# Kernel optimization log

Hardware: AMD Instinct MI355X
Metric: run time of the kernel (lower is better)

The kernel has to match this reference:

```python
import jax, jax.numpy as jnp
import numpy as np

N_NODES = 100000
N_EDGES = 1600000
N_GRAPHS = 1000
X_S = 128
HID = 64


def setup_inputs() -> dict:
    key = jax.random.key(0)
    ks = jax.random.split(key, 12)
    x = jax.random.normal(ks[0], (N_NODES, X_S), dtype=jnp.float32)
    edge_index = jax.random.randint(ks[1], (2, N_EDGES), 0, N_NODES, dtype=jnp.int64)
    batch = jnp.sort(jax.random.randint(ks[2], (N_NODES,), 0, N_GRAPHS, dtype=jnp.int64))
    def lin(k, fin, fout):
        s = 1.0 / np.sqrt(fin)
        kw, kb = jax.random.split(k)
        W = jax.random.uniform(kw, (fin, fout), minval=-s, maxval=s, dtype=jnp.float32)
        b = jax.random.uniform(kb, (fout,), minval=-s, maxval=s, dtype=jnp.float32)
        return W, b
    W1, b1 = lin(ks[3], X_S, HID)
    W2, b2 = lin(ks[4], HID, HID)
    W3, b3 = lin(ks[5], HID, HID)
    Wf, bf = lin(ks[6], HID, 10)
    Wl, bl = lin(ks[7], 10, 1)
    eps1 = jnp.float32(0.37)
    eps2 = jnp.float32(0.72)
    eps3 = jnp.float32(0.11)
    return {"x": x, "edge_index": edge_index, "batch": batch,
            "W1": W1, "b1": b1, "W2": W2, "b2": b2, "W3": W3, "b3": b3,
            "Wf": Wf, "bf": bf, "Wl": Wl, "bl": bl,
            "eps1": eps1, "eps2": eps2, "eps3": eps3}


def _gin_conv(h, src, dst, eps, W, b):
    # GIN: nn((1+eps)*x_i + sum_{j in N(i)} x_j); messages flow src -> dst
    agg = jax.ops.segment_sum(h[src], dst, num_segments=N_NODES)  # [N, d]
    return ((1.0 + eps) * h + agg) @ W + b


def reference(x, edge_index, batch, W1, b1, W2, b2, W3, b3, Wf, bf, Wl, bl,
              eps1, eps2, eps3):
    src, dst = edge_index[0], edge_index[1]
    h = jax.nn.relu(_gin_conv(x, src, dst, eps1, W1, b1))
    h = jax.nn.relu(_gin_conv(h, src, dst, eps2, W2, b2))
    h = jax.nn.relu(_gin_conv(h, src, dst, eps3, W3, b3))
    # global_mean_pool over graph ids
    sums = jax.ops.segment_sum(h, batch, num_segments=N_GRAPHS)        # [G, 64]
    cnts = jax.ops.segment_sum(jnp.ones((N_NODES,), h.dtype), batch,
                               num_segments=N_GRAPHS)                   # [G]
    pooled = sums / jnp.maximum(cnts, 1.0)[:, None]
    out = jax.nn.relu(pooled @ Wf + bf) @ Wl + bl                       # [G, 1]
    return out
```

## Files before the change

### kernel.cpp

```cpp
#include <hip/hip_runtime.h>

#define N_NODES 100000
#define N_EDGES 1600000
#define N_GRAPHS 1000

#define NB_C 391
#define B1   1024
#define CHUNK_E ((N_EDGES + B1 - 1) / B1)
#define MTOT (NB_C * B1)
#define STG_MAX 4736

typedef unsigned int uint32;
typedef unsigned short ushort16;
typedef __attribute__((ext_vector_type(8))) short short8;
typedef __attribute__((ext_vector_type(4))) float f32x4;

static __device__ __forceinline__ ushort16 f2bf(float f) {
    uint32 u = __float_as_uint(f);
    u += 0x7fffu + ((u >> 16) & 1u);
    return (ushort16)(u >> 16);
}
static __device__ __forceinline__ uint32 pk2(float a, float b) {
    return (uint32)f2bf(a) | ((uint32)f2bf(b) << 16);
}
static __device__ __forceinline__ void bf2x(uint32 v, float& lo, float& hi) {
    lo = __uint_as_float(v << 16);
    hi = __uint_as_float(v & 0xffff0000u);
}
static __device__ __forceinline__ void acc8(float* a, uint4 v) {
    float lo, hi;
    bf2x(v.x, lo, hi); a[0] += lo; a[1] += hi;
    bf2x(v.y, lo, hi); a[2] += lo; a[3] += hi;
    bf2x(v.z, lo, hi); a[4] += lo; a[5] += hi;
    bf2x(v.w, lo, hi); a[6] += lo; a[7] += hi;
}

union CV8 { uint4 u; short8 s; };

__global__ __launch_bounds__(256) void convw_kernel(
    const float* __restrict__ W1, const float* __restrict__ W2,
    const float* __restrict__ W3,
    ushort16* __restrict__ W1t, ushort16* __restrict__ W2t,
    ushort16* __restrict__ W3t)
{
    int t = threadIdx.x;
    if (blockIdx.x == 0) {
        for (int i = t; i < 64 * 128; i += 256) {
            int j = i >> 7, k = i & 127;
            W1t[i] = f2bf(W1[k * 64 + j]);
        }
    } else if (blockIdx.x == 1) {
        for (int i = t; i < 64 * 64; i += 256) {
            int j = i >> 6, k = i & 63;
            W2t[i] = f2bf(W2[k * 64 + j]);
        }
    } else {
        for (int i = t; i < 64 * 64; i += 256) {
            int j = i >> 6, k = i & 63;
            W3t[i] = f2bf(W3[k * 64 + j]);
        }
    }
}


__global__ __launch_bounds__(256) void count_kernel(
    const int* __restrict__ dst, int* __restrict__ M)
{
    __shared__ int cnt[NB_C];
    int b = blockIdx.x, t = threadIdx.x;
    for (int q = t; q < NB_C; q += 256) cnt[q] = 0;
    __syncthreads();
    int e0 = b * CHUNK_E;
    int e1 = e0 + CHUNK_E; if (e1 > N_EDGES) e1 = N_EDGES;
    for (int e = e0 + t; e < e1; e += 256)
        atomicAdd(&cnt[dst[e] >> 8], 1);
    __syncthreads();
    for (int q = t; q < NB_C; q += 256) M[q * B1 + b] = cnt[q];
}

#define SCAN_B 1024
#define SCAN_NBLK (MTOT / SCAN_B)

__global__ __launch_bounds__(256) void scanA_kernel(
    const int* __restrict__ in, int* __restrict__ excl, int* __restrict__ bsum)
{
    __shared__ int s[256];
    int b = blockIdx.x, t = threadIdx.x;
    int base = b * SCAN_B + t * 4;
    int v[4];
#pragma unroll
    for (int i = 0; i < 4; ++i) v[i] = (base + i < MTOT) ? in[base + i] : 0;
    int tsum = v[0] + v[1] + v[2] + v[3];
    s[t] = tsum;
    __syncthreads();
    for (int off = 1; off < 256; off <<= 1) {
        int x = (t >= off) ? s[t - off] : 0;
        __syncthreads();
        s[t] += x;
        __syncthreads();
    }
    int run = s[t] - tsum;
#pragma unroll
    for (int i = 0; i < 4; ++i) {
        if (base + i < MTOT) excl[base + i] = run;
        run += v[i];
    }
    if (t == 255) bsum[b] = s[255];
}

__global__ __launch_bounds__(512) void scanB_kernel(int* __restrict__ bsum)
{
    __shared__ int s[512];
    int t = threadIdx.x;
    int v = (t < SCAN_NBLK) ? bsum[t] : 0;
    s[t] = v;
    __syncthreads();
    for (int off = 1; off < 512; off <<= 1) {
        int x = (t >= off) ? s[t - off] : 0;
        __syncthreads();
        s[t] += x;
        __syncthreads();
    }
    if (t < SCAN_NBLK) bsum[t] = s[t] - v;
}

__global__ __launch_bounds__(256) void scanC_kernel(
    const int* __restrict__ excl, const int* __restrict__ bsum,
    int* __restrict__ out)
{
    int b = blockIdx.x, t = threadIdx.x;
    int add = bsum[b];
    int base = b * SCAN_B + t * 4;
#pragma unroll
    for (int i = 0; i < 4; ++i)
        if (base + i < MTOT) out[base + i] = excl[base + i] + add;
}

__global__ __launch_bounds__(256) void scatter_kernel(
    const int* __restrict__ src, const int* __restrict__ dst,
    const int* __restrict__ Ms, uint32* __restrict__ tmp)
{
    __shared__ int cnt[NB_C];
    __shared__ int loc[NB_C];
    __shared__ int cur[NB_C];
    __shared__ int msb[NB_C];
    __shared__ int ssum[256];
    __shared__ uint32 staged[CHUNK_E];
    __shared__ unsigned short bkt[CHUNK_E];
    int b = blockIdx.x, t = threadIdx.x;
    int e0 = b * CHUNK_E;
    int e1 = e0 + CHUNK_E; if (e1 > N_EDGES) e1 = N_EDGES;
    int n = e1 - e0;

    for (int q = t; q < NB_C; q += 256) {
        cnt[q] = 0;
        msb[q] = Ms[q * B1 + b];
    }
    __syncthreads();
    for (int e = e0 + t; e < e1; e += 256)
        atomicAdd(&cnt[dst[e] >> 8], 1);
    __syncthreads();
    int q0 = 2 * t, q1 = 2 * t + 1;
    int c0 = (q0 < NB_C) ? cnt[q0] : 0;
    int c1 = (q1 < NB_C) ? cnt[q1] : 0;
    int pairsum = c0 + c1;
    ssum[t] = pairsum;
    __syncthreads();
    for (int off = 1; off < 256; off <<= 1) {
        int x = (t >= off) ? ssum[t - off] : 0;
        __syncthreads();
        ssum[t] += x;
        __syncthreads();
    }
    int excl = ssum[t] - pairsum;
    if (q0 < NB_C) { loc[q0] = excl; cur[q0] = excl; }
    if (q1 < NB_C) { loc[q1] = excl + c0; cur[q1] = excl + c0; }
    __syncthreads();
    for (int e = e0 + t; e < e1; e += 256) {
        int d = dst[e];
        int q = d >> 8;
        int pos = atomicAdd(&cur[q], 1);
        staged[pos] = ((uint32)(d & 255) << 17) | (uint32)src[e];
        bkt[pos] = (unsigned short)q;
    }
    __syncthreads();
    for (int i = t; i < n; i += 256) {
        int q = bkt[i];
        tmp[msb[q] + (i - loc[q])] = staged[i];
    }
}

__global__ __launch_bounds__(256) void finalize_kernel(
    const uint32* __restrict__ tmp, const int* __restrict__ Ms,
    int* __restrict__ row_off, int* __restrict__ esrc)
{
    __shared__ int cnt[256];
    __shared__ int pref[256];
    __shared__ int cur[256];
    __shared__ uint32 stg[STG_MAX];
    int q = blockIdx.x, t = threadIdx.x;
    int start = Ms[q * B1];
    int end = (q == NB_C - 1) ? N_EDGES : Ms[(q + 1) * B1];
    int seg = end - start;

    cnt[t] = 0;
    __syncthreads();
    for (int e = start + t; e < end; e += 256)
        atomicAdd(&cnt[tmp[e] >> 17], 1);
    __syncthreads();
    pref[t] = cnt[t];
    __syncthreads();
    for (int off = 1; off < 256; off <<= 1) {
        int x = (t >= off) ? pref[t - off] : 0;
        __syncthreads();
        pref[t] += x;
        __syncthreads();
    }
    {
        int excl = pref[t] - cnt[t];
        int node = q * 256 + t;
        if (node < N_NODES) row_off[node] = start + excl;
        cur[t] = excl;
    }
    if (q == 0 && t == 0) row_off[N_NODES] = N_EDGES;
    __syncthreads();
    if (seg <= STG_MAX) {
        for (int e = start + t; e < end; e += 256) {
            uint32 u = tmp[e];
            int pos = atomicAdd(&cur[u >> 17], 1);
            stg[pos] = u & 0x1FFFFu;
        }
        __syncthreads();
        for (int i = t; i < seg; i += 256)
            esrc[start + i] = (int)stg[i];
    } else {
        for (int e = start + t; e < end; e += 256) {
            uint32 u = tmp[e];
            int pos = atomicAdd(&cur[u >> 17], 1);
            esrc[start + pos] = (int)(u & 0x1FFFFu);
        }
    }
}

__global__ __launch_bounds__(256) void gemm1_mfma_kernel(
    const float* __restrict__ x,
    const ushort16* __restrict__ Wt,
    ushort16* __restrict__ y)
{
    int lane = threadIdx.x & 63;
    int wave = threadIdx.x >> 6;
    int col = lane & 15, quad = lane >> 4;
    int node0 = blockIdx.x * 64 + wave * 16;
    int anode = node0 + col;

    short8 a[4];
    if (anode < N_NODES) {
        const float* xr = &x[(size_t)anode * 128 + quad * 8];
#pragma unroll
        for (int s = 0; s < 4; ++s) {
            float4 v0 = *(const float4*)&xr[s * 32];
            float4 v1 = *(const float4*)&xr[s * 32 + 4];
            CV8 cv;
            cv.u = make_uint4(pk2(v0.x, v0.y), pk2(v0.z, v0.w),
                              pk2(v1.x, v1.y), pk2(v1.z, v1.w));
            a[s] = cv.s;
        }
    } else {
        short8 z = {0, 0, 0, 0, 0, 0, 0, 0};
#pragma unroll
        for (int s = 0; s < 4; ++s) a[s] = z;
    }

    f32x4 acc[4];
#pragma unroll
    for (int nt = 0; nt < 4; ++nt)
#pragma unroll
        for (int r = 0; r < 4; ++r) acc[nt][r] = 0.0f;

#pragma unroll
    for (int nt = 0; nt < 4; ++nt) {
        const ushort16* wr = &Wt[(size_t)(nt * 16 + col) * 128 + quad * 8];
#pragma unroll
        for (int s = 0; s < 4; ++s) {
            short8 b = *(const short8*)&wr[s * 32];
            acc[nt] = __builtin_amdgcn_mfma_f32_16x16x32_bf16(a[s], b, acc[nt], 0, 0, 0);
        }
    }

#pragma unroll
    for (int nt = 0; nt < 4; ++nt)
#pragma unroll
        for (int r = 0; r < 4; ++r) {
            int node = node0 + quad * 4 + r;
            if (node < N_NODES)
                y[(size_t)node * 64 + nt * 16 + col] = f2bf(acc[nt][r]);
        }
}

__global__ __launch_bounds__(256) void aggregate_kernel(
    const uint4* __restrict__ y4,
    const int* __restrict__ row_off,
    const int* __restrict__ esrc,
    const float* __restrict__ b,
    const float* __restrict__ eps_p,
    uint4* __restrict__ out4)
{
    int lane = threadIdx.x & 63;
    int wave = threadIdx.x >> 6;
    int grp = lane >> 3;
    int w = lane & 7;
    int node = blockIdx.x * 32 + wave * 8 + grp;

    int s0 = row_off[node], s1 = row_off[node + 1];
    float a[8], c[8];
#pragma unroll
    for (int i = 0; i < 8; ++i) { a[i] = 0.f; c[i] = 0.f; }

    int e = s0;
    for (; e + 3 < s1; e += 4) {
        int i0 = esrc[e];
        int i1 = esrc[e + 1];
        int i2 = esrc[e + 2];
        int i3 = esrc[e + 3];
        uint4 v0 = y4[(size_t)i0 * 8 + w];
        uint4 v1 = y4[(size_t)i1 * 8 + w];
        uint4 v2 = y4[(size_t)i2 * 8 + w];
        uint4 v3 = y4[(size_t)i3 * 8 + w];
        acc8(a, v0);
        acc8(c, v1);
        acc8(a, v2);
        acc8(c, v3);
    }
    for (; e < s1; ++e) {
        uint4 v0 = y4[(size_t)esrc[e] * 8 + w];
        acc8(a, v0);
    }
#pragma unroll
    for (int i = 0; i < 8; ++i) a[i] += c[i];

    uint4 sv = y4[(size_t)node * 8 + w];
    float s[8];
    bf2x(sv.x, s[0], s[1]);
    bf2x(sv.y, s[2], s[3]);
    bf2x(sv.z, s[4], s[5]);
    bf2x(sv.w, s[6], s[7]);
    float ep1 = 1.0f + eps_p[0];
    float4 b0 = *(const float4*)&b[w * 8];
    float4 b1 = *(const float4*)&b[w * 8 + 4];
    float r0 = fmaxf(fmaf(ep1, s[0], a[0]) + b0.x, 0.0f);
    float r1 = fmaxf(fmaf(ep1, s[1], a[1]) + b0.y, 0.0f);
    float r2 = fmaxf(fmaf(ep1, s[2], a[2]) + b0.z, 0.0f);
    float r3 = fmaxf(fmaf(ep1, s[3], a[3]) + b0.w, 0.0f);
    float r4 = fmaxf(fmaf(ep1, s[4], a[4]) + b1.x, 0.0f);
    float r5 = fmaxf(fmaf(ep1, s[5], a[5]) + b1.y, 0.0f);
    float r6 = fmaxf(fmaf(ep1, s[6], a[6]) + b1.z, 0.0f);
    float r7 = fmaxf(fmaf(ep1, s[7], a[7]) + b1.w, 0.0f);
    out4[(size_t)node * 8 + w] =
        make_uint4(pk2(r0, r1), pk2(r2, r3), pk2(r4, r5), pk2(r6, r7));
}

__global__ __launch_bounds__(256) void agg_gemm_fused_kernel(
    const uint4* __restrict__ h4,
    const int* __restrict__ row_off,
    const int* __restrict__ esrc,
    const ushort16* __restrict__ Wt,
    const float* __restrict__ bias,
    const float* __restrict__ eps_p,
    ushort16* __restrict__ hout)
{
    __shared__ __align__(16) ushort16 zl[4][16][72];
    int lane = threadIdx.x & 63;
    int wave = threadIdx.x >> 6;
    int g = lane >> 2;
    int c = lane & 3;
    int node0 = blockIdx.x * 64 + wave * 16;
    if (node0 >= N_NODES) return;
    int node = node0 + g;

    int s0 = row_off[node], s1 = row_off[node + 1];
    float a[16], d[16];
#pragma unroll
    for (int i = 0; i < 16; ++i) { a[i] = 0.f; d[i] = 0.f; }

    const size_t cb = (size_t)c * 2;
    int e = s0;
    for (; e + 3 < s1; e += 4) {
        int i0 = esrc[e];
        int i1 = esrc[e + 1];
        int i2 = esrc[e + 2];
        int i3 = esrc[e + 3];
        uint4 v0a = h4[(size_t)i0 * 8 + cb], v0b = h4[(size_t)i0 * 8 + cb + 1];
        uint4 v1a = h4[(size_t)i1 * 8 + cb], v1b = h4[(size_t)i1 * 8 + cb + 1];
        uint4 v2a = h4[(size_t)i2 * 8 + cb], v2b = h4[(size_t)i2 * 8 + cb + 1];
        uint4 v3a = h4[(size_t)i3 * 8 + cb], v3b = h4[(size_t)i3 * 8 + cb + 1];
        acc8(a, v0a); acc8(a + 8, v0b);
        acc8(d, v1a); acc8(d + 8, v1b);
        acc8(a, v2a); acc8(a + 8, v2b);
        acc8(d, v3a); acc8(d + 8, v3b);
    }
    for (; e < s1; ++e) {
        int i0 = esrc[e];
        uint4 va = h4[(size_t)i0 * 8 + cb], vb = h4[(size_t)i0 * 8 + cb + 1];
        acc8(a, va); acc8(a + 8, vb);
    }
#pragma unroll
    for (int i = 0; i < 16; ++i) a[i] += d[i];

    uint4 sva = h4[(size_t)node * 8 + cb], svb = h4[(size_t)node * 8 + cb + 1];
    float s[16];
    bf2x(sva.x, s[0], s[1]);  bf2x(sva.y, s[2], s[3]);
    bf2x(sva.z, s[4], s[5]);  bf2x(sva.w, s[6], s[7]);
    bf2x(svb.x, s[8], s[9]);  bf2x(svb.y, s[10], s[11]);
    bf2x(svb.z, s[12], s[13]); bf2x(svb.w, s[14], s[15]);
    float ep1 = 1.0f + eps_p[0];
    float z[16];
#pragma unroll
    for (int i = 0; i < 16; ++i) z[i] = fmaf(ep1, s[i], a[i]);

    uint4 pA = make_uint4(pk2(z[0], z[1]), pk2(z[2], z[3]),
                          pk2(z[4], z[5]), pk2(z[6], z[7]));
    uint4 pB = make_uint4(pk2(z[8], z[9]), pk2(z[10], z[11]),
                          pk2(z[12], z[13]), pk2(z[14], z[15]));
    *(uint4*)&zl[wave][g][c * 16] = pA;
    *(uint4*)&zl[wave][g][c * 16 + 8] = pB;

    int col = lane & 15, quad = lane >> 4;
    short8 a0 = *(const short8*)&zl[wave][col][quad * 8];
    short8 a1 = *(const short8*)&zl[wave][col][32 + quad * 8];

    f32x4 acc[4];
#pragma unroll
    for (int nt = 0; nt < 4; ++nt)
#pragma unroll
        for (int r = 0; r < 4; ++r) acc[nt][r] = 0.0f;

#pragma unroll
    for (int nt = 0; nt < 4; ++nt) {
        const ushort16* wr = &Wt[(size_t)(nt * 16 + col) * 64 + quad * 8];
        short8 b0 = *(const short8*)&wr[0];
        short8 b1 = *(const short8*)&wr[32];
        acc[nt] = __builtin_amdgcn_mfma_f32_16x16x32_bf16(a0, b0, acc[nt], 0, 0, 0);
        acc[nt] = __builtin_amdgcn_mfma_f32_16x16x32_bf16(a1, b1, acc[nt], 0, 0, 0);
    }

#pragma unroll
    for (int nt = 0; nt < 4; ++nt) {
        float bl = bias[nt * 16 + col];
#pragma unroll
        for (int r = 0; r < 4; ++r) {
            int nd = node0 + quad * 4 + r;
            hout[(size_t)nd * 64 + nt * 16 + col] =
                f2bf(fmaxf(acc[nt][r] + bl, 0.0f));
        }
    }
}

__global__ __launch_bounds__(256) void pool_head_kernel(
    const uint32* __restrict__ hb,
    const int* __restrict__ batch,
    const float* __restrict__ Wf,
    const float* __restrict__ bfv,
    const float* __restrict__ Wl,
    const float* __restrict__ blv,
    float* __restrict__ out)
{
    __shared__ float red[4][64];
    __shared__ float pooled[64];
    __shared__ float hid[10];
    int g = blockIdx.x;
    int t = threadIdx.x;
    int lo = 0, hi = N_NODES;
    while (lo < hi) { int mid = (lo + hi) >> 1; if (batch[mid] < g) lo = mid + 1; else hi = mid; }
    int start = lo;
    hi = N_NODES;
    while (lo < hi) { int mid = (lo + hi) >> 1; if (batch[mid] < g + 1) lo = mid + 1; else hi = mid; }
    int end = lo;

    int c = t & 63, nl = t >> 6;
    int wd = c >> 1, odd = c & 1;
    float acc = 0.0f;
    for (int i = start + nl; i < end; i += 4) {
        uint32 u = hb[(size_t)i * 32 + wd];
        acc += __uint_as_float(odd ? (u & 0xffff0000u) : (u << 16));
    }
    red[nl][c] = acc;
    __syncthreads();
    if (t < 64) {
        float cnt = (float)(end - start);
        float inv = 1.0f / fmaxf(cnt, 1.0f);
        pooled[t] = (red[0][t] + red[1][t] + red[2][t] + red[3][t]) * inv;
    }
    __syncthreads();
    if (t < 10) {
        float s = bfv[t];
#pragma unroll
        for (int k = 0; k < 64; ++k) s = fmaf(pooled[k], Wf[k * 10 + t], s);
        hid[t] = fmaxf(s, 0.0f);
    }
    __syncthreads();
    if (t == 0) {
        float s = blv[0];
#pragma unroll
        for (int j = 0; j < 10; ++j) s = fmaf(hid[j], Wl[j], s);
        out[g] = s;
    }
}

extern "C" void kernel_launch(void* const* d_in, const int* in_sizes, int n_in,
                              void* d_out, int out_size, void* d_ws, size_t ws_size,
                              hipStream_t stream)
{
    const float* x     = (const float*)d_in[0];
    const int*   ei    = (const int*)  d_in[1];
    const int*   src   = ei;
    const int*   dst   = ei + N_EDGES;
    const int*   batch = (const int*)  d_in[2];
    const float* W1    = (const float*)d_in[3];
    const float* b1    = (const float*)d_in[4];
    const float* W2    = (const float*)d_in[5];
    const float* b2    = (const float*)d_in[6];
    const float* W3    = (const float*)d_in[7];
    const float* b3    = (const float*)d_in[8];
    const float* Wf    = (const float*)d_in[9];
    const float* bfv   = (const float*)d_in[10];
    const float* Wl    = (const float*)d_in[11];
    const float* blv   = (const float*)d_in[12];
    const float* eps1  = (const float*)d_in[13];
    const float* eps2  = (const float*)d_in[14];
    const float* eps3  = (const float*)d_in[15];

    ushort16* ybA = (ushort16*)d_ws;
    ushort16* ybB = ybA + (size_t)N_NODES * 64;
    int*   ints = (int*)(ybB + (size_t)N_NODES * 64);
    int*   M       = ints;
    int*   Mex     = M + MTOT;
    int*   Ms      = Mex + MTOT;
    int*   bsum    = Ms + MTOT;
    int*   row_off = bsum + 512;
    int*   esrc    = row_off + N_NODES + 1;
    uint32* tmp    = (uint32*)(esrc + N_EDGES);
    ushort16* W1t = (ushort16*)(((uintptr_t)(tmp + N_EDGES) + 255) & ~(uintptr_t)255);
    ushort16* W2t = W1t + 64 * 128;
    ushort16* W3t = W2t + 64 * 64;

    const int gemm_blk  = (N_NODES + 63) / 64;
    const int agg_blk   = N_NODES / 32;
    const int fused_blk = (N_NODES + 63) / 64;

    convw_kernel<<<3, 256, 0, stream>>>(W1, W2, W3, W1t, W2t, W3t);

    count_kernel<<<B1, 256, 0, stream>>>(dst, M);
    scanA_kernel<<<SCAN_NBLK, 256, 0, stream>>>(M, Mex, bsum);
    scanB_kernel<<<1, 512, 0, stream>>>(bsum);
    scanC_kernel<<<SCAN_NBLK, 256, 0, stream>>>(Mex, bsum, Ms);
    scatter_kernel<<<B1, 256, 0, stream>>>(src, dst, Ms, tmp);
    finalize_kernel<<<NB_C, 256, 0, stream>>>(tmp, Ms, row_off, esrc);

    gemm1_mfma_kernel<<<gemm_blk, 256, 0, stream>>>(x, W1t, ybA);
    aggregate_kernel<<<agg_blk, 256, 0, stream>>>(
        (const uint4*)ybA, row_off, esrc, b1, eps1, (uint4*)ybB);

    agg_gemm_fused_kernel<<<fused_blk, 256, 0, stream>>>(
        (const uint4*)ybB, row_off, esrc, W2t, b2, eps2, ybA);

    agg_gemm_fused_kernel<<<fused_blk, 256, 0, stream>>>(
        (const uint4*)ybA, row_off, esrc, W3t, b3, eps3, ybB);

    pool_head_kernel<<<N_GRAPHS, 256, 0, stream>>>(
        (const uint32*)ybB, batch, Wf, bfv, Wl, blv, (float*)d_out);
}
```

Measured before the change: 304.7 us.

## Replace per-block bin offsets with global atomic counters and fuse count with first GEMM

The per-block×bin count matrix and its three-kernel scan are replaced by global per-bin atomic counters, a single small scan, and atomic reservation of each block's slot in scatter. The edge-count pass is merged into one launch with the first-layer MFMA GEMM so the two independent workloads share the GPU. This removes several kernel launches and the large count-matrix traffic. In exchange, edge order within a bucket now depends on atomic timing, so float summation order can vary between runs, and a memset is added.

```diff
diff --git a/kernel.cpp b/kernel.cpp
--- a/kernel.cpp
+++ b/kernel.cpp
@@ -7,8 +7,8 @@
 #define NB_C 391
 #define B1   1024
 #define CHUNK_E ((N_EDGES + B1 - 1) / B1)
-#define MTOT (NB_C * B1)
 #define STG_MAX 4736
+#define GEMM_BLK ((N_NODES + 63) / 64)
 
 typedef unsigned int uint32;
 typedef unsigned short ushort16;
@@ -62,57 +62,83 @@
     }
 }
 
-
-__global__ __launch_bounds__(256) void count_kernel(
-    const int* __restrict__ dst, int* __restrict__ M)
-{
-    __shared__ int cnt[NB_C];
+__global__ __launch_bounds__(256) void k1_combined_kernel(
+    const int* __restrict__ dst, int* __restrict__ cnt_g,
+    const float* __restrict__ x, const ushort16* __restrict__ W1t,
+    ushort16* __restrict__ y)
+{
     int b = blockIdx.x, t = threadIdx.x;
-    for (int q = t; q < NB_C; q += 256) cnt[q] = 0;
-    __syncthreads();
-    int e0 = b * CHUNK_E;
-    int e1 = e0 + CHUNK_E; if (e1 > N_EDGES) e1 = N_EDGES;
-    for (int e = e0 + t; e < e1; e += 256)
-        atomicAdd(&cnt[dst[e] >> 8], 1);
-    __syncthreads();
-    for (int q = t; q < NB_C; q += 256) M[q * B1 + b] = cnt[q];
-}
-
-#define SCAN_B 1024
-#define SCAN_NBLK (MTOT / SCAN_B)
-
-__global__ __launch_bounds__(256) void scanA_kernel(
-    const int* __restrict__ in, int* __restrict__ excl, int* __restrict__ bsum)
-{
-    __shared__ int s[256];
-    int b = blockIdx.x, t = threadIdx.x;
-    int base = b * SCAN_B + t * 4;
-    int v[4];
-#pragma unroll
-    for (int i = 0; i < 4; ++i) v[i] = (base + i < MTOT) ? in[base + i] : 0;
-    int tsum = v[0] + v[1] + v[2] + v[3];
-    s[t] = tsum;
-    __syncthreads();
-    for (int off = 1; off < 256; off <<= 1) {
-        int x = (t >= off) ? s[t - off] : 0;
-        __syncthreads();
-        s[t] += x;
-        __syncthreads();
-    }
-    int run = s[t] - tsum;
-#pragma unroll
-    for (int i = 0; i < 4; ++i) {
-        if (base + i < MTOT) excl[base + i] = run;
-        run += v[i];
-    }
-    if (t == 255) bsum[b] = s[255];
-}
-
-__global__ __launch_bounds__(512) void scanB_kernel(int* __restrict__ bsum)
+    if (b < B1) {
+        __shared__ int cnt[NB_C];
+        for (int q = t; q < NB_C; q += 256) cnt[q] = 0;
+        __syncthreads();
+        int e0 = b * CHUNK_E;
+        int e1 = e0 + CHUNK_E; if (e1 > N_EDGES) e1 = N_EDGES;
+        for (int e = e0 + t; e < e1; e += 256)
+            atomicAdd(&cnt[dst[e] >> 8], 1);
+        __syncthreads();
+        for (int q = t; q < NB_C; q += 256)
+            if (cnt[q] > 0) atomicAdd(&cnt_g[q], cnt[q]);
+        return;
+    }
+    {
+        int lane = t & 63;
+        int wave = t >> 6;
+        int col = lane & 15, quad = lane >> 4;
+        int node0 = (b - B1) * 64 + wave * 16;
+        int anode = node0 + col;
+
+        short8 a[4];
+        if (anode < N_NODES) {
+            const float* xr = &x[(size_t)anode * 128 + quad * 8];
+#pragma unroll
+            for (int s = 0; s < 4; ++s) {
+                float4 v0 = *(const float4*)&xr[s * 32];
+                float4 v1 = *(const float4*)&xr[s * 32 + 4];
+                CV8 cv;
+                cv.u = make_uint4(pk2(v0.x, v0.y), pk2(v0.z, v0.w),
+                                  pk2(v1.x, v1.y), pk2(v1.z, v1.w));
+                a[s] = cv.s;
+            }
+        } else {
+            short8 z = {0, 0, 0, 0, 0, 0, 0, 0};
+#pragma unroll
+            for (int s = 0; s < 4; ++s) a[s] = z;
+        }
+
+        f32x4 acc[4];
+#pragma unroll
+        for (int nt = 0; nt < 4; ++nt)
+#pragma unroll
+            for (int r = 0; r < 4; ++r) acc[nt][r] = 0.0f;
+
+#pragma unroll
+        for (int nt = 0; nt < 4; ++nt) {
+            const ushort16* wr = &W1t[(size_t)(nt * 16 + col) * 128 + quad * 8];
+#pragma unroll
+            for (int s = 0; s < 4; ++s) {
+                short8 bb8 = *(const short8*)&wr[s * 32];
+                acc[nt] = __builtin_amdgcn_mfma_f32_16x16x32_bf16(a[s], bb8, acc[nt], 0, 0, 0);
+            }
+        }
+
+#pragma unroll
+        for (int nt = 0; nt < 4; ++nt)
+#pragma unroll
+            for (int r = 0; r < 4; ++r) {
+                int node = node0 + quad * 4 + r;
+                if (node < N_NODES)
+                    y[(size_t)node * 64 + nt * 16 + col] = f2bf(acc[nt][r]);
+            }
+    }
+}
+
+__global__ __launch_bounds__(512) void scan_bins_kernel(
+    const int* __restrict__ cnt_g, int* __restrict__ bstart, int* __restrict__ gcur)
 {
     __shared__ int s[512];
     int t = threadIdx.x;
-    int v = (t < SCAN_NBLK) ? bsum[t] : 0;
+    int v = (t < NB_C) ? cnt_g[t] : 0;
     s[t] = v;
     __syncthreads();
     for (int off = 1; off < 512; off <<= 1) {
@@ -121,24 +147,17 @@
         s[t] += x;
         __syncthreads();
     }
-    if (t < SCAN_NBLK) bsum[t] = s[t] - v;
-}
-
-__global__ __launch_bounds__(256) void scanC_kernel(
-    const int* __restrict__ excl, const int* __restrict__ bsum,
-    int* __restrict__ out)
-{
-    int b = blockIdx.x, t = threadIdx.x;
-    int add = bsum[b];
-    int base = b * SCAN_B + t * 4;
-#pragma unroll
-    for (int i = 0; i < 4; ++i)
-        if (base + i < MTOT) out[base + i] = excl[base + i] + add;
+    if (t < NB_C) {
+        int excl = s[t] - v;
+        bstart[t] = excl;
+        gcur[t] = excl;
+    }
+    if (t == 0) bstart[NB_C] = N_EDGES;
 }
 
 __global__ __launch_bounds__(256) void scatter_kernel(
     const int* __restrict__ src, const int* __restrict__ dst,
-    const int* __restrict__ Ms, uint32* __restrict__ tmp)
+    int* __restrict__ gcur, uint32* __restrict__ tmp)
 {
     __shared__ int cnt[NB_C];
     __shared__ int loc[NB_C];
@@ -152,14 +171,13 @@
     int e1 = e0 + CHUNK_E; if (e1 > N_EDGES) e1 = N_EDGES;
     int n = e1 - e0;
 
-    for (int q = t; q < NB_C; q += 256) {
-        cnt[q] = 0;
-        msb[q] = Ms[q * B1 + b];
-    }
+    for (int q = t; q < NB_C; q += 256) cnt[q] = 0;
     __syncthreads();
     for (int e = e0 + t; e < e1; e += 256)
         atomicAdd(&cnt[dst[e] >> 8], 1);
     __syncthreads();
+    for (int q = t; q < NB_C; q += 256)
+        msb[q] = atomicAdd(&gcur[q], cnt[q]);
     int q0 = 2 * t, q1 = 2 * t + 1;
     int c0 = (q0 < NB_C) ? cnt[q0] : 0;
     int c1 = (q1 < NB_C) ? cnt[q1] : 0;
@@ -191,7 +209,7 @@
 }
 
 __global__ __launch_bounds__(256) void finalize_kernel(
-    const uint32* __restrict__ tmp, const int* __restrict__ Ms,
+    const uint32* __restrict__ tmp, const int* __restrict__ bstart,
     int* __restrict__ row_off, int* __restrict__ esrc)
 {
     __shared__ int cnt[256];
@@ -199,8 +217,8 @@
     __shared__ int cur[256];
     __shared__ uint32 stg[STG_MAX];
     int q = blockIdx.x, t = threadIdx.x;
-    int start = Ms[q * B1];
-    int end = (q == NB_C - 1) ? N_EDGES : Ms[(q + 1) * B1];
+    int start = bstart[q];
+    int end = bstart[q + 1];
     int seg = end - start;
 
     cnt[t] = 0;
@@ -240,61 +258,6 @@
             esrc[start + pos] = (int)(u & 0x1FFFFu);
         }
     }
-}
-
-__global__ __launch_bounds__(256) void gemm1_mfma_kernel(
-    const float* __restrict__ x,
-    const ushort16* __restrict__ Wt,
-    ushort16* __restrict__ y)
-{
-    int lane = threadIdx.x & 63;
-    int wave = threadIdx.x >> 6;
-    int col = lane & 15, quad = lane >> 4;
-    int node0 = blockIdx.x * 64 + wave * 16;
-    int anode = node0 + col;
-
-    short8 a[4];
-    if (anode < N_NODES) {
-        const float* xr = &x[(size_t)anode * 128 + quad * 8];
-#pragma unroll
-        for (int s = 0; s < 4; ++s) {
-            float4 v0 = *(const float4*)&xr[s * 32];
-            float4 v1 = *(const float4*)&xr[s * 32 + 4];
-            CV8 cv;
-            cv.u = make_uint4(pk2(v0.x, v0.y), pk2(v0.z, v0.w),
-                              pk2(v1.x, v1.y), pk2(v1.z, v1.w));
-            a[s] = cv.s;
-        }
-    } else {
-        short8 z = {0, 0, 0, 0, 0, 0, 0, 0};
-#pragma unroll
-        for (int s = 0; s < 4; ++s) a[s] = z;
-    }
-
-    f32x4 acc[4];
-#pragma unroll
-    for (int nt = 0; nt < 4; ++nt)
-#pragma unroll
-        for (int r = 0; r < 4; ++r) acc[nt][r] = 0.0f;
-
-#pragma unroll
-    for (int nt = 0; nt < 4; ++nt) {
-        const ushort16* wr = &Wt[(size_t)(nt * 16 + col) * 128 + quad * 8];
-#pragma unroll
-        for (int s = 0; s < 4; ++s) {
-            short8 b = *(const short8*)&wr[s * 32];
-            acc[nt] = __builtin_amdgcn_mfma_f32_16x16x32_bf16(a[s], b, acc[nt], 0, 0, 0);
-        }
-    }
-
-#pragma unroll
-    for (int nt = 0; nt < 4; ++nt)
-#pragma unroll
-        for (int r = 0; r < 4; ++r) {
-            int node = node0 + quad * 4 + r;
-            if (node < N_NODES)
-                y[(size_t)node * 64 + nt * 16 + col] = f2bf(acc[nt][r]);
-        }
 }
 
 __global__ __launch_bounds__(256) void aggregate_kernel(
@@ -532,31 +495,30 @@
     ushort16* ybA = (ushort16*)d_ws;
     ushort16* ybB = ybA + (size_t)N_NODES * 64;
     int*   ints = (int*)(ybB + (size_t)N_NODES * 64);
-    int*   M       = ints;
-    int*   Mex     = M + MTOT;
-    int*   Ms      = Mex + MTOT;
-    int*   bsum    = Ms + MTOT;
-    int*   row_off = bsum + 512;
+    int*   cnt_g   = ints;
+    int*   bstart  = cnt_g + NB_C;
+    int*   gcur    = bstart + NB_C + 1;
+    int*   row_off = gcur + NB_C;
     int*   esrc    = row_off + N_NODES + 1;
     uint32* tmp    = (uint32*)(esrc + N_EDGES);
     ushort16* W1t = (ushort16*)(((uintptr_t)(tmp + N_EDGES) + 255) & ~(uintptr_t)255);
     ushort16* W2t = W1t + 64 * 128;
     ushort16* W3t = W2t + 64 * 64;
 
-    const int gemm_blk  = (N_NODES + 63) / 64;
     const int agg_blk   = N_NODES / 32;
     const int fused_blk = (N_NODES + 63) / 64;
 
+    hipMemsetAsync(cnt_g, 0, NB_C * sizeof(int), stream);
+
     convw_kernel<<<3, 256, 0, stream>>>(W1, W2, W3, W1t, W2t, W3t);
 
-    count_kernel<<<B1, 256, 0, stream>>>(dst, M);
-    scanA_kernel<<<SCAN_NBLK, 256, 0, stream>>>(M, Mex, bsum);
-    scanB_kernel<<<1, 512, 0, stream>>>(bsum);
-    scanC_kernel<<<SCAN_NBLK, 256, 0, stream>>>(Mex, bsum, Ms);
-    scatter_kernel<<<B1, 256, 0, stream>>>(src, dst, Ms, tmp);
-    finalize_kernel<<<NB_C, 256, 0, stream>>>(tmp, Ms, row_off, esrc);
-
-    gemm1_mfma_kernel<<<gemm_blk, 256, 0, stream>>>(x, W1t, ybA);
+    k1_combined_kernel<<<B1 + GEMM_BLK, 256, 0, stream>>>(
+        dst, cnt_g, x, W1t, ybA);
+
+    scan_bins_kernel<<<1, 512, 0, stream>>>(cnt_g, bstart, gcur);
+    scatter_kernel<<<B1, 256, 0, stream>>>(src, dst, gcur, tmp);
+    finalize_kernel<<<NB_C, 256, 0, stream>>>(tmp, bstart, row_off, esrc);
+
     aggregate_kernel<<<agg_blk, 256, 0, stream>>>(
         (const uint4*)ybA, row_off, esrc, b1, eps1, (uint4*)ybB);
 
```

Result: slower. 346.7 us (+13.8%).
